# Kernel optimization log

Hardware: AMD Instinct MI355X
Metric: run time of the kernel (lower is better)

## Reference

```python
import jax, jax.numpy as jnp
import numpy as np

DIM = 1024
HEADS = 16
HEAD_DIM = DIM // HEADS


def rotate_half(x):
    x1, x2 = jnp.split(x, 2, axis=-1)
    return jnp.concatenate((-x2, x1), axis=-1)


def rope_tables(T, D, dtype=jnp.float32):
    inv_freq = 1.0 / (10000.0 ** (jnp.arange(0, D, 2, dtype=jnp.float32) / D))
    t = jnp.arange(T, dtype=jnp.float32)
    freqs = jnp.einsum('i,j->ij', t, inv_freq)  # [T, D/2]
    emb = jnp.concatenate((freqs, freqs), axis=-1)  # [T, D]
    return emb.astype(dtype), jnp.cos(emb).astype(dtype), jnp.sin(emb).astype(dtype)


def setup_inputs() -> dict:
    key = jax.random.key(0)
    kx, kq, kk, kv, ko = jax.random.split(key, 5)
    B, T = 2, 4096
    scale = 1.0 / np.sqrt(DIM)
    x = jax.random.normal(kx, (B, T, DIM), dtype=jnp.float32)
    wq = jax.random.normal(kq, (DIM, DIM), dtype=jnp.float32) * scale
    wk = jax.random.normal(kk, (DIM, DIM), dtype=jnp.float32) * scale
    wv = jax.random.normal(kv, (DIM, DIM), dtype=jnp.float32) * scale
    wo = jax.random.normal(ko, (DIM, DIM), dtype=jnp.float32) * scale
    return {"x": x, "wq": wq, "wk": wk, "wv": wv, "wo": wo}


def reference(x, wq, wk, wv, wo):
    B, T, C = x.shape
    H, D = HEADS, HEAD_DIM
    # projections; nn.Linear applies x @ W^T
    q = (x @ wq.T).reshape(B, T, H, D).transpose(0, 2, 1, 3)  # [B,H,T,D]
    k = (x @ wk.T).reshape(B, T, H, D).transpose(0, 2, 1, 3)
    v = (x @ wv.T).reshape(B, T, H, D).transpose(0, 2, 1, 3)
    _, cos, sin = rope_tables(T, D, x.dtype)
    cos = cos[None, None]  # [1,1,T,D]
    sin = sin[None, None]
    q = q * cos + rotate_half(q) * sin
    k = k * cos + rotate_half(k) * sin
    scores = jnp.einsum('bhtd,bhsd->bhts', q, k) / jnp.sqrt(jnp.asarray(D, x.dtype))
    attn = jax.nn.softmax(scores, axis=-1)
    out = jnp.einsum('bhts,bhsd->bhtd', attn, v)
    out = out.transpose(0, 2, 1, 3).reshape(B, T, C)
    return out @ wo.T
```

## Files before the change

kernel.cpp:

```cpp
#include <hip/hip_runtime.h>
#include <hip/hip_bf16.h>
#include <math.h>


typedef __attribute__((ext_vector_type(8))) short short8;
typedef __attribute__((ext_vector_type(4))) short short4v;
typedef __attribute__((ext_vector_type(4))) float floatx4;

using bf16 = __hip_bfloat16;

static constexpr int T_ = 4096;
static constexpr int C_ = 1024;
static constexpr int M_ = 8192;
static constexpr float QSCALE = 0.125f * 1.44269504088896340736f;

#if __has_builtin(__builtin_amdgcn_mfma_f32_16x16x16bf16_1k)
#define USE_K16 1
#else
#define USE_K16 0
#endif

#if __has_builtin(__builtin_amdgcn_exp2f)
#define EXP2 __builtin_amdgcn_exp2f
#else
#define EXP2 exp2f
#endif

__device__ __forceinline__ floatx4 mfma16(short8 a, short8 b, floatx4 c) {
    return __builtin_amdgcn_mfma_f32_16x16x32_bf16(a, b, c, 0, 0, 0);
}
#if USE_K16
__device__ __forceinline__ floatx4 mfma_k16(short4v a, short4v b, floatx4 c) {
    return __builtin_amdgcn_mfma_f32_16x16x16bf16_1k(a, b, c, 0, 0, 0);
}
#endif

__device__ __forceinline__ short8 ld8(const bf16* p) {
    return *reinterpret_cast<const short8*>(p);
}
__device__ __forceinline__ short4v ld4(const bf16* p) {
    return *reinterpret_cast<const short4v*>(p);
}
__device__ __forceinline__ void st8(bf16* p, short8 v) {
    *reinterpret_cast<short8*>(p) = v;
}
__device__ __forceinline__ unsigned short f2bf(float x) {
    bf16 h = __float2bfloat16(x);
    return reinterpret_cast<unsigned short&>(h);
}

__device__ __forceinline__ int pack2bf(float a, float b, unsigned sel) {
    const unsigned ua = __float_as_uint(a) + 0x8000u;
    const unsigned ub = __float_as_uint(b) + 0x8000u;
    int r;
    asm("v_perm_b32 %0, %1, %2, %3" : "=v"(r) : "v"(ub), "v"(ua), "s"(sel));
    return r;
}
__device__ __forceinline__ short4v i2s4(int lo, int hi) {
    union { int2 i; short4v s; } u;
    u.i.x = lo; u.i.y = hi;
    return u.s;
}
__device__ __forceinline__ short8 i2s8(int a, int b, int c, int d) {
    union { int4 i; short8 s; } u;
    u.i.x = a; u.i.y = b; u.i.z = c; u.i.w = d;
    return u.s;
}

__device__ __forceinline__ void cp16(const bf16* g, bf16* l) {
    __builtin_amdgcn_global_load_lds(
        (const __attribute__((address_space(1))) void*)g,
        (__attribute__((address_space(3))) void*)l, 16, 0, 0);
}

__global__ __launch_bounds__(256)
void cvt_kernel(const float* __restrict__ in, bf16* __restrict__ out, int n8) {
    const int i = blockIdx.x * blockDim.x + threadIdx.x;
    if (i >= n8) return;
    const float4* p = reinterpret_cast<const float4*>(in) + (size_t)i * 2;
    const float4 a = p[0];
    const float4 b = p[1];
    short8 v;
    v[0] = (short)f2bf(a.x); v[1] = (short)f2bf(a.y);
    v[2] = (short)f2bf(a.z); v[3] = (short)f2bf(a.w);
    v[4] = (short)f2bf(b.x); v[5] = (short)f2bf(b.y);
    v[6] = (short)f2bf(b.z); v[7] = (short)f2bf(b.w);
    *(reinterpret_cast<short8*>(out) + i) = v;
}

__global__ __launch_bounds__(256)
void cvt4_kernel(const float* __restrict__ p0, const float* __restrict__ p1,
                 const float* __restrict__ p2, const float* __restrict__ p3,
                 bf16* __restrict__ out) {
    const int i   = blockIdx.x * blockDim.x + threadIdx.x;
    const int seg = i >> 17;
    const int off = i & 131071;
    const float* in = (seg == 0) ? p0 : (seg == 1) ? p1 : (seg == 2) ? p2 : p3;
    const float4* p = reinterpret_cast<const float4*>(in) + (size_t)off * 2;
    const float4 a = p[0];
    const float4 b = p[1];
    short8 v;
    v[0] = (short)f2bf(a.x); v[1] = (short)f2bf(a.y);
    v[2] = (short)f2bf(a.z); v[3] = (short)f2bf(a.w);
    v[4] = (short)f2bf(b.x); v[5] = (short)f2bf(b.y);
    v[6] = (short)f2bf(b.z); v[7] = (short)f2bf(b.w);
    *(reinterpret_cast<short8*>(out) + i) = v;
}

__global__ __launch_bounds__(256)
void rope_table_kernel(float2* __restrict__ CS) {
    const int i = blockIdx.x * blockDim.x + threadIdx.x;
    const int t = i >> 5;
    const int j = i & 31;
    const float inv_freq = expf(-(float)j * 0.28782313662425575f);
    float s, c;
    sincosf((float)t * inv_freq, &s, &c);
    CS[i] = make_float2(c, s);
}

__global__ __launch_bounds__(256)
void gemm128_kernel(const bf16* __restrict__ A, const bf16* __restrict__ W,
                    void* __restrict__ out, int mode) {
    const int m0   = blockIdx.x * 128;
    const int n0   = blockIdx.y * 128;
    const int tid  = threadIdx.x;
    const int lane = tid & 63;
    const int wave = tid >> 6;
    const int quad = lane >> 4;
    const int lr   = lane & 15;
    const int wr   = (wave >> 1) * 64;
    const int wc   = (wave & 1) * 64;

    __shared__ __align__(16) bf16 Als[2][128 * 32];
    __shared__ __align__(16) bf16 Bls[2][128 * 32];

    const int srow = tid >> 2;
    const int scol = (tid & 3) * 8;

    floatx4 acc[4][4];
#pragma unroll
    for (int i = 0; i < 4; ++i)
#pragma unroll
        for (int j = 0; j < 4; ++j) acc[i][j] = floatx4{0.f, 0.f, 0.f, 0.f};

    const bf16* Ab = A + (size_t)m0 * C_;
    const bf16* Wb = W + (size_t)n0 * C_;

#pragma unroll
    for (int j = 0; j < 2; ++j) {
        const int row = srow + j * 64;
        cp16(Ab + (size_t)row * C_ + scol, &Als[0][(j * 256 + tid) * 8]);
        cp16(Wb + (size_t)row * C_ + scol, &Bls[0][(j * 256 + tid) * 8]);
    }
    __syncthreads();

    for (int k = 0; k < C_; k += 32) {
        const int buf = (k >> 5) & 1;
        if (k + 32 < C_) {
            const int nb = buf ^ 1;
#pragma unroll
            for (int j = 0; j < 2; ++j) {
                const int row = srow + j * 64;
                cp16(Ab + (size_t)row * C_ + k + 32 + scol,
                     &Als[nb][(j * 256 + tid) * 8]);
                cp16(Wb + (size_t)row * C_ + k + 32 + scol,
                     &Bls[nb][(j * 256 + tid) * 8]);
            }
        }

        short8 a[4], b[4];
#pragma unroll
        for (int i = 0; i < 4; ++i)
            a[i] = ld8(&Als[buf][(wr + i * 16 + lr) * 32 + quad * 8]);
#pragma unroll
        for (int j = 0; j < 4; ++j)
            b[j] = ld8(&Bls[buf][(wc + j * 16 + lr) * 32 + quad * 8]);
#pragma unroll
        for (int i = 0; i < 4; ++i)
#pragma unroll
            for (int j = 0; j < 4; ++j) acc[i][j] = mfma16(a[i], b[j], acc[i][j]);

        __syncthreads();
    }

    if (mode == 0) {
        bf16* ob = (bf16*)out;
#pragma unroll
        for (int j = 0; j < 4; ++j) {
            const int col = n0 + wc + j * 16 + lr;
#pragma unroll
            for (int i = 0; i < 4; ++i)
#pragma unroll
                for (int r = 0; r < 4; ++r) {
                    const int m = m0 + wr + i * 16 + quad * 4 + r;
                    ob[(size_t)m * C_ + col] = __float2bfloat16(acc[i][j][r]);
                }
        }
    } else if (mode == 1) {
        unsigned short* ob = (unsigned short*)out;
        const int b2 = m0 >> 12;
#pragma unroll
        for (int j = 0; j < 4; ++j) {
            const int n = n0 + wc + j * 16 + lr;
            const int h = n >> 6;
            const int d = n & 63;
#pragma unroll
            for (int i = 0; i < 4; ++i) {
                const int t0 = (m0 & 4095) + wr + i * 16 + quad * 4;
                ushort4 v;
                v.x = f2bf(acc[i][j][0]); v.y = f2bf(acc[i][j][1]);
                v.z = f2bf(acc[i][j][2]); v.w = f2bf(acc[i][j][3]);
                size_t idx = ((size_t)((b2 * 16 + h) * 64 + d)) * T_ + t0;
                *reinterpret_cast<ushort4*>(ob + idx) = v;
            }
        }
    } else {
        float* of = (float*)out;
#pragma unroll
        for (int j = 0; j < 4; ++j) {
            const int col = n0 + wc + j * 16 + lr;
#pragma unroll
            for (int i = 0; i < 4; ++i)
#pragma unroll
                for (int r = 0; r < 4; ++r) {
                    const int m = m0 + wr + i * 16 + quad * 4 + r;
                    of[(size_t)m * C_ + col] = acc[i][j][r];
                }
        }
    }
}

__global__ __launch_bounds__(256)
void gemm_qkv_kernel(const bf16* __restrict__ A, const bf16* __restrict__ W,
                     bf16* __restrict__ Qbase, const float2* __restrict__ CS) {
    const int m0   = blockIdx.x * 128;
    const int n0g  = blockIdx.y * 128;
    const int tid  = threadIdx.x;
    const int lane = tid & 63;
    const int wave = tid >> 6;
    const int quad = lane >> 4;
    const int lr   = lane & 15;
    const int wr   = (wave >> 1) * 64;
    const int wc   = (wave & 1) * 64;

    __shared__ __align__(16) bf16 Als[2][128 * 32];
    __shared__ __align__(16) bf16 Bls[2][128 * 32];

    const int srow = tid >> 2;
    const int scol = (tid & 3) * 8;

    floatx4 acc[4][4];
#pragma unroll
    for (int i = 0; i < 4; ++i)
#pragma unroll
        for (int j = 0; j < 4; ++j) acc[i][j] = floatx4{0.f, 0.f, 0.f, 0.f};

    const bf16* Ab = A + (size_t)m0 * C_;
    const bf16* Wb = W + (size_t)n0g * C_;

#pragma unroll
    for (int j = 0; j < 2; ++j) {
        const int row = srow + j * 64;
        cp16(Ab + (size_t)row * C_ + scol, &Als[0][(j * 256 + tid) * 8]);
        cp16(Wb + (size_t)row * C_ + scol, &Bls[0][(j * 256 + tid) * 8]);
    }
    __syncthreads();

    for (int k = 0; k < C_; k += 32) {
        const int buf = (k >> 5) & 1;
        if (k + 32 < C_) {
            const int nb = buf ^ 1;
#pragma unroll
            for (int j = 0; j < 2; ++j) {
                const int row = srow + j * 64;
                cp16(Ab + (size_t)row * C_ + k + 32 + scol,
                     &Als[nb][(j * 256 + tid) * 8]);
                cp16(Wb + (size_t)row * C_ + k + 32 + scol,
                     &Bls[nb][(j * 256 + tid) * 8]);
            }
        }

        short8 a[4], b[4];
#pragma unroll
        for (int i = 0; i < 4; ++i)
            a[i] = ld8(&Als[buf][(wr + i * 16 + lr) * 32 + quad * 8]);
#pragma unroll
        for (int j = 0; j < 4; ++j)
            b[j] = ld8(&Bls[buf][(wc + j * 16 + lr) * 32 + quad * 8]);
#pragma unroll
        for (int i = 0; i < 4; ++i)
#pragma unroll
            for (int j = 0; j < 4; ++j) acc[i][j] = mfma16(a[i], b[j], acc[i][j]);

        __syncthreads();
    }

    const int seg = n0g >> 10;
    const int n0  = n0g & 1023;
    if (seg < 2) {
        bf16* ob = Qbase + (size_t)seg * M_ * C_;
        const float scale = (seg == 0) ? QSCALE : 1.0f;
        const int tb = (m0 & 4095) + wr + quad * 4;
#pragma unroll
        for (int j = 0; j < 2; ++j) {
            const int col  = n0 + wc + j * 16 + lr;
            const int jcol = j * 16 + lr;
#pragma unroll
            for (int i = 0; i < 4; ++i) {
#pragma unroll
                for (int r = 0; r < 4; ++r) {
                    const int t = tb + i * 16 + r;
                    const float2 cs = CS[t * 32 + jcol];
                    const float q1 = acc[i][j][r];
                    const float q2 = acc[i][j + 2][r];
                    const int m = m0 + wr + i * 16 + quad * 4 + r;
                    ob[(size_t)m * C_ + col] =
                        __float2bfloat16((q1 * cs.x - q2 * cs.y) * scale);
                    ob[(size_t)m * C_ + col + 32] =
                        __float2bfloat16((q2 * cs.x + q1 * cs.y) * scale);
                }
            }
        }
    } else {
        unsigned short* ob = (unsigned short*)(Qbase + (size_t)2 * M_ * C_);
        const int b2 = m0 >> 12;
#pragma unroll
        for (int j = 0; j < 4; ++j) {
            const int n = n0 + wc + j * 16 + lr;
            const int h = n >> 6;
            const int d = n & 63;
#pragma unroll
            for (int i = 0; i < 4; ++i) {
                const int t0 = (m0 & 4095) + wr + i * 16 + quad * 4;
                ushort4 v;
                v.x = f2bf(acc[i][j][0]); v.y = f2bf(acc[i][j][1]);
                v.z = f2bf(acc[i][j][2]); v.w = f2bf(acc[i][j][3]);
                size_t idx = ((size_t)((b2 * 16 + h) * 64 + d)) * T_ + t0;
                *reinterpret_cast<ushort4*>(ob + idx) = v;
            }
        }
    }
}

__global__ __launch_bounds__(256)
void attn_kernel(const bf16* __restrict__ Q, const bf16* __restrict__ K,
                 const bf16* __restrict__ Vt, bf16* __restrict__ AO) {
    const int tid  = threadIdx.x;
    const int lane = tid & 63;
    const int wave = tid >> 6;
    const int quad = lane >> 4;
    const int lr   = lane & 15;
    const int bh   = blockIdx.y;
    const int b    = bh >> 4;
    const int h    = bh & 15;
    const int q0   = blockIdx.x * 128 + wave * 32;

    const bf16* Qb = Q + (size_t)b * T_ * C_ + h * 64;
    const bf16* Kb = K + (size_t)b * T_ * C_ + h * 64;
    const bf16* Vb = Vt + (size_t)bh * 64 * T_;

#if USE_K16
    __shared__ __align__(16) bf16 Kls[2][64 * 64];
    __shared__ __align__(16) bf16 Vls[2][64 * 64];

    const int srow  = tid >> 3;
    const int sc    = tid & 7;
    const int sphys = (sc ^ (srow & 7)) * 8;
    const int soff0 = srow * 64 + sphys;
    const int soff1 = (srow + 32) * 64 + sphys;

    const unsigned psel = 0x07060302u;
    const floatx4 FZ = {0.f, 0.f, 0.f, 0.f};
    const int one2 = 0x3F803F80;
    const short8 VONE = i2s8(one2, one2, one2, one2);

    short8 aq[2][2];
#pragma unroll
    for (int t = 0; t < 2; ++t) {
        aq[t][0] = ld8(Qb + (size_t)(q0 + t * 16 + lr) * C_ + quad * 8);
        aq[t][1] = ld8(Qb + (size_t)(q0 + t * 16 + lr) * C_ + 32 + quad * 8);
    }

    floatx4 O[2][4];
#pragma unroll
    for (int t = 0; t < 2; ++t)
#pragma unroll
        for (int dt = 0; dt < 4; ++dt) O[t][dt] = floatx4{0.f, 0.f, 0.f, 0.f};
    floatx4 Osum[2] = {{0.f, 0.f, 0.f, 0.f}, {0.f, 0.f, 0.f, 0.f}};

    const int lr7    = lr & 7;
    const int kchunk = (quad ^ lr7) * 8;
    const int vsub   = (quad & 1) * 4;
    const int vbq    = quad >> 1;
    const int kel0   = lr * 64 + kchunk;
    const int kel1   = kel0 ^ 32;
    int velk[4];
#pragma unroll
    for (int kk = 0; kk < 4; ++kk)
        velk[kk] = lr * 64 + (((2 * kk + vbq) ^ lr7) * 8) + vsub;

    short8 kr0, kr1, vr0, vr1;
#define LOAD_STAGE(kv0)                                              \
    do {                                                             \
        kr0 = ld8(Kb + (size_t)((kv0) + srow) * C_ + sc * 8);        \
        kr1 = ld8(Kb + (size_t)((kv0) + srow + 32) * C_ + sc * 8);   \
        vr0 = ld8(Vb + (size_t)srow * T_ + (kv0) + sc * 8);          \
        vr1 = ld8(Vb + (size_t)(srow + 32) * T_ + (kv0) + sc * 8);   \
    } while (0)
#define STORE_STAGE(p)                                               \
    do {                                                             \
        st8(&Kls[p][soff0], kr0);                                    \
        st8(&Kls[p][soff1], kr1);                                    \
        st8(&Vls[p][soff0], vr0);                                    \
        st8(&Vls[p][soff1], vr1);                                    \
    } while (0)

#define BAR()                                                        \
    do {                                                             \
        asm volatile("s_waitcnt lgkmcnt(0)" ::: "memory");           \
        __builtin_amdgcn_s_barrier();                                \
    } while (0)

#define COMPUTE(P)                                                            \
    do {                                                                      \
        const bf16* Ks = Kls[P];                                              \
        const bf16* Vs = Vls[P];                                              \
        int prlo[2][4], prhi[2][4];                                           \
        _Pragma("unroll")                                                     \
        for (int kk = 0; kk < 4; ++kk) {                                      \
            const short8 kf0 = ld8(Ks + kk * 1024 + kel0);                    \
            const short8 kf1 = ld8(Ks + kk * 1024 + kel1);                    \
            floatx4 s0 = mfma16(kf0, aq[0][0], FZ);                           \
            s0 = mfma16(kf1, aq[0][1], s0);                                   \
            floatx4 s1 = mfma16(kf0, aq[1][0], FZ);                           \
            s1 = mfma16(kf1, aq[1][1], s1);                                   \
            const float e0 = EXP2(s0[0]), e1 = EXP2(s0[1]);                   \
            const float e2 = EXP2(s0[2]), e3 = EXP2(s0[3]);                   \
            prlo[0][kk] = pack2bf(e0, e1, psel);                              \
            prhi[0][kk] = pack2bf(e2, e3, psel);                              \
            const float f0 = EXP2(s1[0]), f1 = EXP2(s1[1]);                   \
            const float f2 = EXP2(s1[2]), f3 = EXP2(s1[3]);                   \
            prlo[1][kk] = pack2bf(f0, f1, psel);                              \
            prhi[1][kk] = pack2bf(f2, f3, psel);                              \
        }                                                                     \
        \
        Osum[0] = mfma16(i2s8(prlo[0][0], prhi[0][0], prlo[0][1], prhi[0][1]),\
                         VONE, Osum[0]);                                      \
        Osum[0] = mfma16(i2s8(prlo[0][2], prhi[0][2], prlo[0][3], prhi[0][3]),\
                         VONE, Osum[0]);                                      \
        Osum[1] = mfma16(i2s8(prlo[1][0], prhi[1][0], prlo[1][1], prhi[1][1]),\
                         VONE, Osum[1]);                                      \
        Osum[1] = mfma16(i2s8(prlo[1][2], prhi[1][2], prlo[1][3], prhi[1][3]),\
                         VONE, Osum[1]);                                      \
        __builtin_amdgcn_s_setprio(1);                                        \
        _Pragma("unroll")                                                     \
        for (int dt = 0; dt < 4; ++dt) {                                      \
            _Pragma("unroll")                                                 \
            for (int kk = 0; kk < 4; ++kk) {                                  \
                const short4v vf = ld4(Vs + dt * 1024 + velk[kk]);            \
                O[0][dt] = mfma_k16(i2s4(prlo[0][kk], prhi[0][kk]), vf, O[0][dt]); \
                O[1][dt] = mfma_k16(i2s4(prlo[1][kk], prhi[1][kk]), vf, O[1][dt]); \
            }                                                                 \
        }                                                                     \
        __builtin_amdgcn_s_setprio(0);                                        \
    } while (0)

    LOAD_STAGE(0);
    STORE_STAGE(0);
    LOAD_STAGE(64);
    BAR();

    constexpr int NS = T_ / 64;
    for (int s = 0; s < NS; s += 2) {
        if (s + 1 < NS) STORE_STAGE(1);
        if (s + 2 < NS) LOAD_STAGE((s + 2) * 64);
        COMPUTE(0);
        BAR();
        if (s + 2 < NS) STORE_STAGE(0);
        if (s + 3 < NS) LOAD_STAGE((s + 3) * 64);
        COMPUTE(1);
        BAR();
    }

#pragma unroll
    for (int t = 0; t < 2; ++t) {
#pragma unroll
        for (int r = 0; r < 4; ++r) {
            const float inv = 1.0f / fmaxf(Osum[t][r], 1e-30f);
            const size_t row =
                (size_t)(b * T_ + q0 + t * 16 + quad * 4 + r) * C_ + h * 64;
            AO[row + 0  + lr] = __float2bfloat16(O[t][0][r] * inv);
            AO[row + 16 + lr] = __float2bfloat16(O[t][1][r] * inv);
            AO[row + 32 + lr] = __float2bfloat16(O[t][2][r] * inv);
            AO[row + 48 + lr] = __float2bfloat16(O[t][3][r] * inv);
        }
    }
#undef LOAD_STAGE
#undef STORE_STAGE
#undef COMPUTE
#undef BAR
#else
    __shared__ __align__(16) unsigned short Pbuf[4][512];
    unsigned short* Pw = Pbuf[wave];
    for (int half = 0; half < 2; ++half) {
        const int qh = q0 + half * 16;
        const short8 aq0 = ld8(Qb + (size_t)(qh + lr) * C_ + quad * 8);
        const short8 aq1 = ld8(Qb + (size_t)(qh + lr) * C_ + 32 + quad * 8);
        floatx4 O0 = {0,0,0,0}, O1 = {0,0,0,0}, O2 = {0,0,0,0}, O3 = {0,0,0,0};
        float lrun[4] = {0.f, 0.f, 0.f, 0.f};
        for (int kv = 0; kv < T_; kv += 32) {
            floatx4 S0 = {0,0,0,0}, S1 = {0,0,0,0};
            const bf16* k0 = Kb + (size_t)(kv + lr) * C_ + quad * 8;
            const bf16* k1 = Kb + (size_t)(kv + 16 + lr) * C_ + quad * 8;
            S0 = mfma16(aq0, ld8(k0), S0);
            S0 = mfma16(aq1, ld8(k0 + 32), S0);
            S1 = mfma16(aq0, ld8(k1), S1);
            S1 = mfma16(aq1, ld8(k1 + 32), S1);
#pragma unroll
            for (int r = 0; r < 4; ++r) {
                const float e0 = exp2f(S0[r]);
                const float e1 = exp2f(S1[r]);
                lrun[r] += e0 + e1;
                const int row = quad * 4 + r;
                Pw[row * 32 + lr]      = f2bf(e0);
                Pw[row * 32 + 16 + lr] = f2bf(e1);
            }
            __syncthreads();
            const short8 ap = *reinterpret_cast<const short8*>(Pw + lr * 32 + quad * 8);
            O0 = mfma16(ap, ld8(Vb + (size_t)(lr)      * T_ + kv + quad * 8), O0);
            O1 = mfma16(ap, ld8(Vb + (size_t)(16 + lr) * T_ + kv + quad * 8), O1);
            O2 = mfma16(ap, ld8(Vb + (size_t)(32 + lr) * T_ + kv + quad * 8), O2);
            O3 = mfma16(ap, ld8(Vb + (size_t)(48 + lr) * T_ + kv + quad * 8), O3);
            __syncthreads();
        }
#pragma unroll
        for (int r = 0; r < 4; ++r) {
            float l = lrun[r];
            l += __shfl_xor(l, 1); l += __shfl_xor(l, 2);
            l += __shfl_xor(l, 4); l += __shfl_xor(l, 8);
            const float inv = 1.0f / fmaxf(l, 1e-30f);
            const size_t row = (size_t)(b * T_ + qh + quad * 4 + r) * C_ + h * 64;
            AO[row + 0  + lr] = __float2bfloat16(O0[r] * inv);
            AO[row + 16 + lr] = __float2bfloat16(O1[r] * inv);
            AO[row + 32 + lr] = __float2bfloat16(O2[r] * inv);
            AO[row + 48 + lr] = __float2bfloat16(O3[r] * inv);
        }
    }
#endif
}

extern "C" void kernel_launch(void* const* d_in, const int* in_sizes, int n_in,
                              void* d_out, int out_size, void* d_ws, size_t ws_size,
                              hipStream_t stream) {
    const float* x  = (const float*)d_in[0];
    const float* wq = (const float*)d_in[1];
    const float* wk = (const float*)d_in[2];
    const float* wv = (const float*)d_in[3];
    const float* wo = (const float*)d_in[4];
    float* out = (float*)d_out;

    bf16* xb  = (bf16*)d_ws;
    bf16* wqb = xb  + (size_t)M_ * C_;
    bf16* wkb = wqb + (size_t)C_ * C_;
    bf16* wvb = wkb + (size_t)C_ * C_;
    bf16* wob = wvb + (size_t)C_ * C_;
    bf16* Q   = wob + (size_t)C_ * C_;
    bf16* K   = Q   + (size_t)M_ * C_;
    bf16* Vt  = K   + (size_t)M_ * C_;
    float2* CS = (float2*)(Vt + (size_t)M_ * C_);
    bf16* AO  = xb;

    rope_table_kernel<<<(T_ * 32) / 256, 256, 0, stream>>>(CS);
    cvt_kernel<<<(M_ * C_ / 8 + 255) / 256, 256, 0, stream>>>(x, xb, M_ * C_ / 8);
    cvt4_kernel<<<(4 * C_ * C_ / 8) / 256, 256, 0, stream>>>(wq, wk, wv, wo, wqb);

    gemm_qkv_kernel<<<dim3(M_ / 128, 24), dim3(256), 0, stream>>>(xb, wqb, Q, CS);

    attn_kernel<<<dim3(T_ / 128, 32), 256, 0, stream>>>(Q, K, Vt, AO);

    gemm128_kernel<<<dim3(M_ / 128, C_ / 128), dim3(256), 0, stream>>>(AO, wob, out, 2);
}
```

Baseline: 393.1 us.

## Merge prep kernels into one launch and swizzle GEMM block order for XCD locality

Replaces the three preprocessing launches (x cast, weight casts, RoPE table) with a single prep kernel that dispatches on block index. The QKV and output-projection GEMMs switch to a 1D grid whose block index is remapped so that blocks landing on the same XCD (orig & 7) work on contiguous M rows. This is meant to improve L2 reuse of the A tiles on MI355X's chiplet layout and to save launch overhead. It also drops the unused mode-1 epilogue.

Measured after the change: 392.8 us. About the same (-0.1%).

```diff
diff --git a/kernel.cpp b/kernel.cpp
--- a/kernel.cpp
+++ b/kernel.cpp
@@ -74,55 +74,54 @@
 }
 
 __global__ __launch_bounds__(256)
-void cvt_kernel(const float* __restrict__ in, bf16* __restrict__ out, int n8) {
-    const int i = blockIdx.x * blockDim.x + threadIdx.x;
-    if (i >= n8) return;
-    const float4* p = reinterpret_cast<const float4*>(in) + (size_t)i * 2;
-    const float4 a = p[0];
-    const float4 b = p[1];
-    short8 v;
-    v[0] = (short)f2bf(a.x); v[1] = (short)f2bf(a.y);
-    v[2] = (short)f2bf(a.z); v[3] = (short)f2bf(a.w);
-    v[4] = (short)f2bf(b.x); v[5] = (short)f2bf(b.y);
-    v[6] = (short)f2bf(b.z); v[7] = (short)f2bf(b.w);
-    *(reinterpret_cast<short8*>(out) + i) = v;
-}
-
-__global__ __launch_bounds__(256)
-void cvt4_kernel(const float* __restrict__ p0, const float* __restrict__ p1,
-                 const float* __restrict__ p2, const float* __restrict__ p3,
-                 bf16* __restrict__ out) {
-    const int i   = blockIdx.x * blockDim.x + threadIdx.x;
-    const int seg = i >> 17;
-    const int off = i & 131071;
-    const float* in = (seg == 0) ? p0 : (seg == 1) ? p1 : (seg == 2) ? p2 : p3;
-    const float4* p = reinterpret_cast<const float4*>(in) + (size_t)off * 2;
-    const float4 a = p[0];
-    const float4 b = p[1];
-    short8 v;
-    v[0] = (short)f2bf(a.x); v[1] = (short)f2bf(a.y);
-    v[2] = (short)f2bf(a.z); v[3] = (short)f2bf(a.w);
-    v[4] = (short)f2bf(b.x); v[5] = (short)f2bf(b.y);
-    v[6] = (short)f2bf(b.z); v[7] = (short)f2bf(b.w);
-    *(reinterpret_cast<short8*>(out) + i) = v;
-}
-
-__global__ __launch_bounds__(256)
-void rope_table_kernel(float2* __restrict__ CS) {
-    const int i = blockIdx.x * blockDim.x + threadIdx.x;
-    const int t = i >> 5;
-    const int j = i & 31;
-    const float inv_freq = expf(-(float)j * 0.28782313662425575f);
-    float s, c;
-    sincosf((float)t * inv_freq, &s, &c);
-    CS[i] = make_float2(c, s);
+void prep_kernel(const float* __restrict__ x,
+                 const float* __restrict__ wq, const float* __restrict__ wk,
+                 const float* __restrict__ wv, const float* __restrict__ wo,
+                 bf16* __restrict__ xb, bf16* __restrict__ wqb,
+                 float2* __restrict__ CS) {
+    const int blk = blockIdx.x;
+    if (blk < 6144) {
+        const float* in;
+        bf16* out;
+        int i;
+        if (blk < 4096) {
+            i = blk * 256 + threadIdx.x;
+            in = x; out = xb;
+        } else {
+            i = (blk - 4096) * 256 + threadIdx.x;
+            const int seg = i >> 17;
+            const int off = i & 131071;
+            in = (seg == 0) ? wq : (seg == 1) ? wk : (seg == 2) ? wv : wo;
+            out = wqb + (size_t)i * 8 - (size_t)off * 8;
+            i = off;
+        }
+        const float4* p = reinterpret_cast<const float4*>(in) + (size_t)i * 2;
+        const float4 a = p[0];
+        const float4 b = p[1];
+        short8 v;
+        v[0] = (short)f2bf(a.x); v[1] = (short)f2bf(a.y);
+        v[2] = (short)f2bf(a.z); v[3] = (short)f2bf(a.w);
+        v[4] = (short)f2bf(b.x); v[5] = (short)f2bf(b.y);
+        v[6] = (short)f2bf(b.z); v[7] = (short)f2bf(b.w);
+        *(reinterpret_cast<short8*>(out) + i) = v;
+    } else {
+        const int i = (blk - 6144) * 256 + threadIdx.x;
+        const int t = i >> 5;
+        const int j = i & 31;
+        const float inv_freq = expf(-(float)j * 0.28782313662425575f);
+        float s, c;
+        sincosf((float)t * inv_freq, &s, &c);
+        CS[i] = make_float2(c, s);
+    }
 }
 
 __global__ __launch_bounds__(256)
 void gemm128_kernel(const bf16* __restrict__ A, const bf16* __restrict__ W,
-                    void* __restrict__ out, int mode) {
-    const int m0   = blockIdx.x * 128;
-    const int n0   = blockIdx.y * 128;
+                    void* __restrict__ out, int mode, int ntile, int cpx) {
+    const int orig = blockIdx.x;
+    const int swz  = (orig & 7) * cpx + (orig >> 3);
+    const int m0   = (swz / ntile) * 128;
+    const int n0   = (swz % ntile) * 128;
     const int tid  = threadIdx.x;
     const int lane = tid & 63;
     const int wave = tid >> 6;
@@ -196,24 +195,6 @@
                     ob[(size_t)m * C_ + col] = __float2bfloat16(acc[i][j][r]);
                 }
         }
-    } else if (mode == 1) {
-        unsigned short* ob = (unsigned short*)out;
-        const int b2 = m0 >> 12;
-#pragma unroll
-        for (int j = 0; j < 4; ++j) {
-            const int n = n0 + wc + j * 16 + lr;
-            const int h = n >> 6;
-            const int d = n & 63;
-#pragma unroll
-            for (int i = 0; i < 4; ++i) {
-                const int t0 = (m0 & 4095) + wr + i * 16 + quad * 4;
-                ushort4 v;
-                v.x = f2bf(acc[i][j][0]); v.y = f2bf(acc[i][j][1]);
-                v.z = f2bf(acc[i][j][2]); v.w = f2bf(acc[i][j][3]);
-                size_t idx = ((size_t)((b2 * 16 + h) * 64 + d)) * T_ + t0;
-                *reinterpret_cast<ushort4*>(ob + idx) = v;
-            }
-        }
     } else {
         float* of = (float*)out;
 #pragma unroll
@@ -233,8 +214,10 @@
 __global__ __launch_bounds__(256)
 void gemm_qkv_kernel(const bf16* __restrict__ A, const bf16* __restrict__ W,
                      bf16* __restrict__ Qbase, const float2* __restrict__ CS) {
-    const int m0   = blockIdx.x * 128;
-    const int n0g  = blockIdx.y * 128;
+    const int orig = blockIdx.x;
+    const int swz  = (orig & 7) * 192 + (orig >> 3);
+    const int m0   = (swz / 24) * 128;
+    const int n0g  = (swz % 24) * 128;
     const int tid  = threadIdx.x;
     const int lane = tid & 63;
     const int wave = tid >> 6;
@@ -570,13 +553,11 @@
     float2* CS = (float2*)(Vt + (size_t)M_ * C_);
     bf16* AO  = xb;
 
-    rope_table_kernel<<<(T_ * 32) / 256, 256, 0, stream>>>(CS);
-    cvt_kernel<<<(M_ * C_ / 8 + 255) / 256, 256, 0, stream>>>(x, xb, M_ * C_ / 8);
-    cvt4_kernel<<<(4 * C_ * C_ / 8) / 256, 256, 0, stream>>>(wq, wk, wv, wo, wqb);
-
-    gemm_qkv_kernel<<<dim3(M_ / 128, 24), dim3(256), 0, stream>>>(xb, wqb, Q, CS);
+    prep_kernel<<<6656, 256, 0, stream>>>(x, wq, wk, wv, wo, xb, wqb, CS);
+
+    gemm_qkv_kernel<<<1536, 256, 0, stream>>>(xb, wqb, Q, CS);
 
     attn_kernel<<<dim3(T_ / 128, 32), 256, 0, stream>>>(Q, K, Vt, AO);
 
-    gemm128_kernel<<<dim3(M_ / 128, C_ / 128), dim3(256), 0, stream>>>(AO, wob, out, 2);
-}
+    gemm128_kernel<<<512, 256, 0, stream>>>(AO, wob, out, 2, 8, 64);
+}
```
